# Kernel tuning notes

Hardware: AMD Instinct MI355X
Metric: run time of the kernel (lower is better)

## Reference

```python
import jax, jax.numpy as jnp
import numpy as np

N, S, E, D = 20000, 4096, 640000, 256
SPARSITY = 0.02  # fraction of nonzero entries in the normalized matrix


def setup_inputs() -> dict:
    key = jax.random.key(0)
    ks = jax.random.split(key, 6)
    u = jax.random.uniform(ks[0], (N, S), dtype=jnp.float32)
    init = jnp.where(u < SPARSITY, u, 0.0)
    edge_index = jax.random.randint(ks[1], (2, E), 0, N, dtype=jnp.int32)
    edge_attr = jax.random.uniform(ks[2], (E,), dtype=jnp.float32)
    # Projection MLP params (Linear(1,16) -> ReLU -> Linear(16,D))
    w1 = jax.random.normal(ks[3], (1, 16), dtype=jnp.float32)
    b1 = jnp.zeros((16,), dtype=jnp.float32)
    w2 = jax.random.normal(ks[4], (16, D), dtype=jnp.float32) / np.float32(np.sqrt(16))
    b2 = jnp.zeros((D,), dtype=jnp.float32)
    # GCN weight (xavier-ish)
    W = jax.random.normal(ks[5], (D, D), dtype=jnp.float32) / np.float32(np.sqrt(D))
    return {"init": init, "edge_index": edge_index, "edge_attr": edge_attr,
            "w1": w1, "b1": b1, "w2": w2, "b2": b2, "W": W}


def reference(init, edge_index, edge_attr, w1, b1, w2, b2, W):
    n, s = init.shape
    # Projection: torch code feeds the nonzero COLUMN INDICES (as floats) of each
    # row through the MLP and means them. Vectorized: precompute MLP(j) for all
    # column indices j, then do a masked mean via a single matmul.
    idx = jnp.arange(s, dtype=init.dtype)[:, None]          # [S,1]
    phi = jax.nn.relu(idx @ w1 + b1) @ w2 + b2              # [S,D]
    mask = (init != 0).astype(init.dtype)                   # [N,S]
    cnt = mask.sum(axis=1)                                  # [N]
    # rows with zero nonzeros yield zero embedding (matches torch branch)
    h = (mask @ phi) / jnp.maximum(cnt, 1.0)[:, None]       # [N,D]

    # 3-layer GCN: scatter_add of h[row]*attr into col, then mm + relu
    row, col = edge_index[0], edge_index[1]
    for _ in range(3):
        h_agg = jax.ops.segment_sum(h[row] * edge_attr[:, None], col,
                                    num_segments=n)          # [N,D]
        h = jax.nn.relu(h_agg @ W)
    return h
```

## Files before the change

kernel.cpp:

```cpp
#include <hip/hip_runtime.h>


#define N_NODES 20000
#define S_COLS  4096
#define E_EDGES 640000
#define D_DIM   256

typedef unsigned short bf16_t;
typedef __attribute__((ext_vector_type(8))) short short8;
typedef __attribute__((ext_vector_type(4))) float f32x4;

__device__ __forceinline__ float bf2f(bf16_t u) {
    union { unsigned int i; float f; } v; v.i = ((unsigned int)u) << 16; return v.f;
}
__device__ __forceinline__ bf16_t f2bf(float x) {
    union { float f; unsigned int i; } v; v.f = x;
    unsigned int r = v.i + 0x7FFF + ((v.i >> 16) & 1);
    return (bf16_t)(r >> 16);
}
__device__ __forceinline__ float lo_bf(unsigned int u) {
    union { unsigned int i; float f; } v; v.i = u << 16; return v.f;
}
__device__ __forceinline__ float hi_bf(unsigned int u) {
    union { unsigned int i; float f; } v; v.i = u & 0xFFFF0000u; return v.f;
}
__device__ __forceinline__ unsigned int pack_bf(float a, float b) {
    return (unsigned int)f2bf(a) | ((unsigned int)f2bf(b) << 16);
}

__global__ void __launch_bounds__(256, 4)
mega_kernel(const float* __restrict__ init_m,
            const float* __restrict__ w1, const float* __restrict__ b1,
            const float* __restrict__ w2, const float* __restrict__ b2,
            bf16_t* __restrict__ h,
            const int* __restrict__ eidx, int* __restrict__ cnt,
            const float* __restrict__ W,
            bf16_t* __restrict__ Wt_hi, bf16_t* __restrict__ Wt_lo) {
    int b = blockIdx.x;
    int t = threadIdx.x;

    if (b >= 5000) {
        int bb = b - 5000;
        if (bb < 2500) {
            int e = bb * 256 + t;
            atomicAdd(&cnt[eidx[E_EDGES + e]], 1);
        } else {
            int k = bb - 2500;
            float w = W[k * D_DIM + t];
            bf16_t hi = f2bf(w);
            bf16_t lo = f2bf(w - bf2f(hi));
            Wt_hi[t * D_DIM + k] = hi;
            Wt_lo[t * D_DIM + k] = lo;
        }
        return;
    }

    __shared__ float w2s[16][256];
#pragma unroll
    for (int k = 0; k < 16; ++k) w2s[k][t] = w2[k * D_DIM + t];
    __syncthreads();

    int wave = t >> 6, lane = t & 63;
    int row  = b * 4 + wave;

    float lw1[16], lb1[16];
#pragma unroll
    for (int k = 0; k < 16; ++k) { lw1[k] = w1[k]; lb1[k] = b1[k]; }

    const float4* rowp = (const float4*)(init_m + (size_t)row * S_COLS);
    float f[16] = {};
    float cn = 0.f;

#define PROC_COMP(val, jb)                                            \
    if ((val) != 0.f) {                                               \
        float jf = (float)(jb);                                       \
        _Pragma("unroll")                                             \
        for (int k = 0; k < 16; ++k)                                  \
            f[k] += fmaxf(jf * lw1[k] + lb1[k], 0.f);                 \
        cn += 1.f;                                                    \
    }

#pragma unroll 4
    for (int v = 0; v < 16; ++v) {
        float4 x = rowp[v * 64 + lane];
        int jb = (v * 64 + lane) * 4;
        PROC_COMP(x.x, jb)
        PROC_COMP(x.y, jb + 1)
        PROC_COMP(x.z, jb + 2)
        PROC_COMP(x.w, jb + 3)
    }
#undef PROC_COMP

#pragma unroll
    for (int off = 32; off > 0; off >>= 1) {
#pragma unroll
        for (int k = 0; k < 16; ++k) f[k] += __shfl_xor(f[k], off, 64);
        cn += __shfl_xor(cn, off, 64);
    }

    float4 b2v = *(const float4*)(b2 + 4 * lane);
    float o0 = cn * b2v.x, o1 = cn * b2v.y, o2 = cn * b2v.z, o3 = cn * b2v.w;
#pragma unroll
    for (int k = 0; k < 16; ++k) {
        float4 wv = *(const float4*)(&w2s[k][4 * lane]);
        o0 += f[k] * wv.x;  o1 += f[k] * wv.y;
        o2 += f[k] * wv.z;  o3 += f[k] * wv.w;
    }
    float inv = 1.f / fmaxf(cn, 1.f);
    uint2 o;
    o.x = pack_bf(o0 * inv, o1 * inv);
    o.y = pack_bf(o2 * inv, o3 * inv);
    *(uint2*)(h + (size_t)row * D_DIM + 4 * lane) = o;
}

__global__ void scan_kernel(const int* __restrict__ cnt, int* __restrict__ offs,
                            int* __restrict__ cur) {
    __shared__ int sdata[1024];
    int t = threadIdx.x;
    int base = t * 20;
    int vals[20];
    int local = 0;
#pragma unroll
    for (int k = 0; k < 20; ++k) {
        int idx = base + k;
        int v = (idx < N_NODES) ? cnt[idx] : 0;
        vals[k] = local;
        local += v;
    }
    sdata[t] = local;
    __syncthreads();
    for (int off = 1; off < 1024; off <<= 1) {
        int v = (t >= off) ? sdata[t - off] : 0;
        __syncthreads();
        sdata[t] += v;
        __syncthreads();
    }
    int prefix = (t == 0) ? 0 : sdata[t - 1];
#pragma unroll
    for (int k = 0; k < 20; ++k) {
        int idx = base + k;
        if (idx < N_NODES) {
            int o = prefix + vals[k];
            offs[idx] = o;
            cur[idx]  = o;
        }
    }
    if (t == 1023) offs[N_NODES] = sdata[1023];
}

__global__ void fill_kernel(const int* __restrict__ eidx, const float* __restrict__ attr,
                            int* __restrict__ cur, int* __restrict__ src_s,
                            float* __restrict__ attr_s) {
    int e = blockIdx.x * 256 + threadIdx.x;
    if (e < E_EDGES) {
        int r = eidx[e];
        int c = eidx[E_EDGES + e];
        int pos = atomicAdd(&cur[c], 1);
        src_s[pos]  = r;
        attr_s[pos] = attr[e];
    }
}

__global__ void gather_kernel(const bf16_t* __restrict__ h,
                              const int* __restrict__ offs,
                              const int* __restrict__ src_s,
                              const float* __restrict__ attr_s,
                              bf16_t* __restrict__ g) {
    int wid  = (blockIdx.x * blockDim.x + threadIdx.x) >> 6;
    int lane = threadIdx.x & 63;
    if (wid >= N_NODES) return;
    int half = lane >> 5;
    int l32  = lane & 31;
    int e0 = offs[wid], e1 = offs[wid + 1];

    float acc[8] = {};
    for (int base = e0; base < e1; base += 64) {
        int n = e1 - base; if (n > 64) n = 64;
        int   r_l = 0; float a_l = 0.f;
        if (lane < n) { r_l = src_s[base + lane]; a_l = attr_s[base + lane]; }
        int nn = (n + 15) & ~15;
        for (int q = 0; q < nn; q += 16) {
#pragma unroll
            for (int u = 0; u < 8; ++u) {
                int   sl = q + 2 * u + half;
                int   r  = __shfl(r_l, sl, 64);
                float a  = __shfl(a_l, sl, 64);
                uint4 v  = ((const uint4*)(h + (size_t)r * D_DIM))[l32];
                acc[0] += lo_bf(v.x) * a;  acc[1] += hi_bf(v.x) * a;
                acc[2] += lo_bf(v.y) * a;  acc[3] += hi_bf(v.y) * a;
                acc[4] += lo_bf(v.z) * a;  acc[5] += hi_bf(v.z) * a;
                acc[6] += lo_bf(v.w) * a;  acc[7] += hi_bf(v.w) * a;
            }
        }
    }
#pragma unroll
    for (int i = 0; i < 8; ++i) acc[i] += __shfl_xor(acc[i], 32, 64);

    if (half == 0) {
        uint4 o;
        o.x = pack_bf(acc[0], acc[1]);
        o.y = pack_bf(acc[2], acc[3]);
        o.z = pack_bf(acc[4], acc[5]);
        o.w = pack_bf(acc[6], acc[7]);
        ((uint4*)(g + (size_t)wid * D_DIM))[l32] = o;
    }
}

__global__ void __launch_bounds__(256, 2)
gemm_relu_kernel(const bf16_t* __restrict__ g,
                 const bf16_t* __restrict__ Wt_hi,
                 const bf16_t* __restrict__ Wt_lo,
                 bf16_t* __restrict__ hdst, float* __restrict__ fdst) {
    __shared__ bf16_t Bs[64][512];
    int tid  = threadIdx.x;
    int w    = tid >> 6;
    int lane = tid & 63;
    int quad = lane >> 4;
    int id16 = lane & 15;
    int bn   = blockIdx.y * 64;
    int bm0  = blockIdx.x * 160;

    char* bs = (char*)Bs;

    {
        int tn0 = tid >> 4;
        int ts0 = tid & 15;
#pragma unroll
        for (int it = 0; it < 16; ++it) {
            int n   = tn0 + (it & 3) * 16;
            int seg = ts0 + (it >> 2) * 16;
            const bf16_t* src = (seg < 32 ? Wt_hi : Wt_lo)
                              + (size_t)(bn + n) * D_DIM + (seg & 31) * 8;
            unsigned off = (unsigned)(n * 1024 + seg * 16) ^ (unsigned)((n & 7) << 4);
            *(uint4*)(bs + off) = *(const uint4*)src;
        }
    }

    int r0 = bm0 + w * 16;
    const bf16_t* arow = g + (size_t)(r0 + id16) * D_DIM;
    short8 areg[8];
#pragma unroll
    for (int i = 0; i < 8; ++i)
        areg[i] = *(const short8*)(arow + i * 32 + quad * 8);

    __syncthreads();

    unsigned swz   = (unsigned)((id16 & 7) << 4);
    unsigned nbase = (unsigned)(id16 * 1024);

    for (int t = w; t < 10; t += 4) {
        short8 anext[8];
        int tn = t + 4;
        if (tn < 10) {
            const bf16_t* an = g + (size_t)(bm0 + tn * 16 + id16) * D_DIM;
#pragma unroll
            for (int i = 0; i < 8; ++i)
                anext[i] = *(const short8*)(an + i * 32 + quad * 8);
        }

        f32x4 acc[4];
#pragma unroll
        for (int nt = 0; nt < 4; ++nt) acc[nt] = (f32x4){0.f, 0.f, 0.f, 0.f};

#pragma unroll
        for (int ks = 0; ks < 8; ++ks) {
            short8 a = areg[ks];
            unsigned kb = ((unsigned)(ks * 64 + quad * 16)) ^ swz;
#pragma unroll
            for (int nt = 0; nt < 4; ++nt) {
                unsigned off = (unsigned)(nt * 16384) + nbase + kb;
                short8 bh = *(const short8*)(bs + off);
                short8 bl = *(const short8*)(bs + off + 512);
                acc[nt] = __builtin_amdgcn_mfma_f32_16x16x32_bf16(a, bh, acc[nt], 0, 0, 0);
                acc[nt] = __builtin_amdgcn_mfma_f32_16x16x32_bf16(a, bl, acc[nt], 0, 0, 0);
            }
        }

        int mrow = bm0 + t * 16;
#pragma unroll
        for (int nt = 0; nt < 4; ++nt) {
#pragma unroll
            for (int r = 0; r < 4; ++r) {
                int m = mrow + quad * 4 + r;
                int n = bn + nt * 16 + id16;
                float v = fmaxf(acc[nt][r], 0.f);
                if (hdst) hdst[(size_t)m * D_DIM + n] = f2bf(v);
                else      fdst[(size_t)m * D_DIM + n] = v;
            }
        }
#pragma unroll
        for (int i = 0; i < 8; ++i) areg[i] = anext[i];
    }
}

extern "C" void kernel_launch(void* const* d_in, const int* in_sizes, int n_in,
                              void* d_out, int out_size, void* d_ws, size_t ws_size,
                              hipStream_t stream) {
    const float* init_m = (const float*)d_in[0];
    const int*   eidx   = (const int*)  d_in[1];
    const float* attr   = (const float*)d_in[2];
    const float* w1     = (const float*)d_in[3];
    const float* b1     = (const float*)d_in[4];
    const float* w2     = (const float*)d_in[5];
    const float* b2     = (const float*)d_in[6];
    const float* Wm     = (const float*)d_in[7];
    float* out = (float*)d_out;

    char* ws = (char*)d_ws;
    bf16_t* hbuf   = (bf16_t*)ws;
    bf16_t* gbuf   = (bf16_t*)(ws + 10240000);
    int*    cnt    = (int*)   (ws + 20529152);
    int*    offs   = (int*)   (ws + 20609152);
    int*    cur    = (int*)   (ws + 20689408);
    int*    src_s  = (int*)   (ws + 20769408);
    float*  attr_s = (float*) (ws + 23329408);
    bf16_t* Wt_hi  = (bf16_t*)(ws + 25889408);
    bf16_t* Wt_lo  = (bf16_t*)(ws + 26020480);

    hipMemsetAsync(ws + 20480000, 0, 129152, stream);

    mega_kernel<<<5000 + 2500 + 256, 256, 0, stream>>>(
        init_m, w1, b1, w2, b2, hbuf, eidx, cnt, Wm, Wt_hi, Wt_lo);
    scan_kernel<<<1, 1024, 0, stream>>>(cnt, offs, cur);
    fill_kernel<<<(E_EDGES + 255) / 256, 256, 0, stream>>>(eidx, attr, cur, src_s, attr_s);

    dim3 ggrid((N_NODES * 64 + 255) / 256);
    dim3 mgrid(125, 4);
    for (int it = 0; it < 3; ++it) {
        gather_kernel<<<ggrid, 256, 0, stream>>>(hbuf, offs, src_s, attr_s, gbuf);
        if (it == 2)
            gemm_relu_kernel<<<mgrid, 256, 0, stream>>>(gbuf, Wt_hi, Wt_lo,
                                                        (bf16_t*)nullptr, out);
        else
            gemm_relu_kernel<<<mgrid, 256, 0, stream>>>(gbuf, Wt_hi, Wt_lo,
                                                        hbuf, (float*)nullptr);
    }
}
```

Before: 761.5 us.

## Retile GEMM so each wave computes two row tiles, with XCD-aware block remap

The GEMM+ReLU kernel now uses 128-row blocks in which each wave computes two 16-row tiles at once. Each B fragment read from LDS is reused across two MFMA row tiles, replacing the sequential per-wave tile loop and its register prefetch. A 1D grid of 628 blocks is remapped so that consecutive logical tiles land on the same XCD, aiming for better L2 locality. The last block reads rows past N from the workspace, but stores are guarded; the change also raises register pressure.

```diff
diff --git a/kernel.cpp b/kernel.cpp
--- a/kernel.cpp
+++ b/kernel.cpp
@@ -217,8 +217,15 @@
     int lane = tid & 63;
     int quad = lane >> 4;
     int id16 = lane & 15;
-    int bn   = blockIdx.y * 64;
-    int bm0  = blockIdx.x * 160;
+
+    int d    = blockIdx.x;
+    int xcd  = d & 7;
+    int base = (xcd < 4) ? xcd * 79 : 316 + (xcd - 4) * 78;
+    int wg   = base + (d >> 3);
+    int bx   = wg >> 2;
+    int by   = wg & 3;
+    int bn   = by * 64;
+    int bm0  = bx * 128;
 
     char* bs = (char*)Bs;
 
@@ -236,60 +243,57 @@
         }
     }
 
-    int r0 = bm0 + w * 16;
-    const bf16_t* arow = g + (size_t)(r0 + id16) * D_DIM;
-    short8 areg[8];
-#pragma unroll
-    for (int i = 0; i < 8; ++i)
-        areg[i] = *(const short8*)(arow + i * 32 + quad * 8);
+    int r0 = bm0 + w * 32;
+    short8 areg[2][8];
+#pragma unroll
+    for (int j = 0; j < 2; ++j) {
+        const bf16_t* arow = g + (size_t)(r0 + j * 16 + id16) * D_DIM;
+#pragma unroll
+        for (int i = 0; i < 8; ++i)
+            areg[j][i] = *(const short8*)(arow + i * 32 + quad * 8);
+    }
 
     __syncthreads();
 
     unsigned swz   = (unsigned)((id16 & 7) << 4);
     unsigned nbase = (unsigned)(id16 * 1024);
 
-    for (int t = w; t < 10; t += 4) {
-        short8 anext[8];
-        int tn = t + 4;
-        if (tn < 10) {
-            const bf16_t* an = g + (size_t)(bm0 + tn * 16 + id16) * D_DIM;
-#pragma unroll
-            for (int i = 0; i < 8; ++i)
-                anext[i] = *(const short8*)(an + i * 32 + quad * 8);
-        }
-
-        f32x4 acc[4];
-#pragma unroll
-        for (int nt = 0; nt < 4; ++nt) acc[nt] = (f32x4){0.f, 0.f, 0.f, 0.f};
-
-#pragma unroll
-        for (int ks = 0; ks < 8; ++ks) {
-            short8 a = areg[ks];
-            unsigned kb = ((unsigned)(ks * 64 + quad * 16)) ^ swz;
-#pragma unroll
-            for (int nt = 0; nt < 4; ++nt) {
-                unsigned off = (unsigned)(nt * 16384) + nbase + kb;
-                short8 bh = *(const short8*)(bs + off);
-                short8 bl = *(const short8*)(bs + off + 512);
-                acc[nt] = __builtin_amdgcn_mfma_f32_16x16x32_bf16(a, bh, acc[nt], 0, 0, 0);
-                acc[nt] = __builtin_amdgcn_mfma_f32_16x16x32_bf16(a, bl, acc[nt], 0, 0, 0);
+    f32x4 acc[2][4];
+#pragma unroll
+    for (int j = 0; j < 2; ++j)
+#pragma unroll
+        for (int nt = 0; nt < 4; ++nt) acc[j][nt] = (f32x4){0.f, 0.f, 0.f, 0.f};
+
+#pragma unroll
+    for (int ks = 0; ks < 8; ++ks) {
+        unsigned kb = ((unsigned)(ks * 64 + quad * 16)) ^ swz;
+#pragma unroll
+        for (int nt = 0; nt < 4; ++nt) {
+            unsigned off = (unsigned)(nt * 16384) + nbase + kb;
+            short8 bh = *(const short8*)(bs + off);
+            short8 bl = *(const short8*)(bs + off + 512);
+            acc[0][nt] = __builtin_amdgcn_mfma_f32_16x16x32_bf16(areg[0][ks], bh, acc[0][nt], 0, 0, 0);
+            acc[0][nt] = __builtin_amdgcn_mfma_f32_16x16x32_bf16(areg[0][ks], bl, acc[0][nt], 0, 0, 0);
+            acc[1][nt] = __builtin_amdgcn_mfma_f32_16x16x32_bf16(areg[1][ks], bh, acc[1][nt], 0, 0, 0);
+            acc[1][nt] = __builtin_amdgcn_mfma_f32_16x16x32_bf16(areg[1][ks], bl, acc[1][nt], 0, 0, 0);
+        }
+    }
+
+#pragma unroll
+    for (int j = 0; j < 2; ++j) {
+#pragma unroll
+        for (int nt = 0; nt < 4; ++nt) {
+#pragma unroll
+            for (int r = 0; r < 4; ++r) {
+                int m = r0 + j * 16 + quad * 4 + r;
+                if (m < N_NODES) {
+                    int n = bn + nt * 16 + id16;
+                    float v = fmaxf(acc[j][nt][r], 0.f);
+                    if (hdst) hdst[(size_t)m * D_DIM + n] = f2bf(v);
+                    else      fdst[(size_t)m * D_DIM + n] = v;
+                }
             }
         }
-
-        int mrow = bm0 + t * 16;
-#pragma unroll
-        for (int nt = 0; nt < 4; ++nt) {
-#pragma unroll
-            for (int r = 0; r < 4; ++r) {
-                int m = mrow + quad * 4 + r;
-                int n = bn + nt * 16 + id16;
-                float v = fmaxf(acc[nt][r], 0.f);
-                if (hdst) hdst[(size_t)m * D_DIM + n] = f2bf(v);
-                else      fdst[(size_t)m * D_DIM + n] = v;
-            }
-        }
-#pragma unroll
-        for (int i = 0; i < 8; ++i) areg[i] = anext[i];
     }
 }
 
@@ -325,14 +329,13 @@
     fill_kernel<<<(E_EDGES + 255) / 256, 256, 0, stream>>>(eidx, attr, cur, src_s, attr_s);
 
     dim3 ggrid((N_NODES * 64 + 255) / 256);
-    dim3 mgrid(125, 4);
     for (int it = 0; it < 3; ++it) {
         gather_kernel<<<ggrid, 256, 0, stream>>>(hbuf, offs, src_s, attr_s, gbuf);
         if (it == 2)
-            gemm_relu_kernel<<<mgrid, 256, 0, stream>>>(gbuf, Wt_hi, Wt_lo,
-                                                        (bf16_t*)nullptr, out);
+            gemm_relu_kernel<<<628, 256, 0, stream>>>(gbuf, Wt_hi, Wt_lo,
+                                                      (bf16_t*)nullptr, out);
         else
-            gemm_relu_kernel<<<mgrid, 256, 0, stream>>>(gbuf, Wt_hi, Wt_lo,
-                                                        hbuf, (float*)nullptr);
-    }
-}
+            gemm_relu_kernel<<<628, 256, 0, stream>>>(gbuf, Wt_hi, Wt_lo,
+                                                      hbuf, (float*)nullptr);
+    }
+}
```

Result: faster. 694.3 us (-8.8%).
